# Kernel optimization log

Measured on AMD Instinct MI355X. Metric: run time of the kernel, lower is better.

Reference implementation:

```python
import jax, jax.numpy as jnp
import numpy as np

EPS = 1e-8

def div_safe(n, d):
    return n / jnp.maximum(d, EPS)

def cos_sim(v1, v2):
    # torch F.cosine_similarity along last axis (broadcasting allowed)
    n1 = jnp.linalg.norm(v1, axis=-1)
    n2 = jnp.linalg.norm(v2, axis=-1)
    dot = jnp.sum(v1 * v2, axis=-1)
    return dot / (jnp.maximum(n1, EPS) * jnp.maximum(n2, EPS))

def cosine_pairwise(v1, v2):
    # v1: (B,L1,H), v2: (B,L2,H) -> (B,L1,L2)
    n1 = jnp.linalg.norm(v1, axis=2)[:, :, None]        # (B,L1,1)
    n2 = jnp.linalg.norm(v2, axis=2)[:, None, :]        # (B,1,L2)
    a = jnp.einsum('bih,bjh->bij', v1, v2)
    return div_safe(a, n1 * n2)

def mpm(v1, v2, w):
    # v1: (B,L,H); v2: (B,L,H) or (B,1,H) (broadcast); w: (P,H)
    mv1 = cos_sim(v1, v2)[..., None]                     # (B,L,1)
    v1w = w[None, None] * v1[:, :, None, :]              # (B,L,P,H)
    v2w = w[None, None] * v2[:, :, None, :]              # (B,L or 1,P,H)
    mvp = cos_sim(v1w, v2w)                              # (B,L,P)
    return [mv1, mvp]

def mpm_pairwise(v1, v2, w):
    # v1: (B,L1,H), v2: (B,L2,H), w: (P,H) -> (B,L1,L2,P)
    v1w = w[None, :, None, :] * v1[:, None, :, :]        # (B,P,L1,H)
    v2w = w[None, :, None, :] * v2[:, None, :, :]        # (B,P,L2,H)
    n = jnp.einsum('bpih,bpjh->bpij', v1w, v2w)
    n1 = jnp.linalg.norm(v1w, axis=3)[:, :, :, None]     # (B,P,L1,1)
    n2 = jnp.linalg.norm(v2w, axis=3)[:, :, None, :]     # (B,P,1,L2)
    return div_safe(n, n1 * n2).transpose(0, 2, 3, 1)

def matching_forward(context_p, mask_p, context_h, mask_h, params):
    H = params.shape[-1]
    B = context_p.shape[0]
    p_fw, p_bw = context_p[..., :H], context_p[..., H:]
    h_fw, h_bw = context_h[..., :H], context_h[..., H:]

    len_p = jnp.sum(mask_p, axis=1)
    len_h = jnp.sum(mask_h, axis=1)
    last_p = jnp.clip(len_p - 1, 0)
    last_h = jnp.clip(len_h - 1, 0)
    bidx = jnp.arange(B)
    p_fw_last = p_fw[bidx, last_p][:, None, :]           # (B,1,H)
    h_fw_last = h_fw[bidx, last_h][:, None, :]
    p_bw_last = p_bw[:, 0:1, :]
    h_bw_last = h_bw[:, 0:1, :]

    cos_fw = cosine_pairwise(p_fw, h_fw)                 # (B,L1,L2)
    cos_bw = cosine_pairwise(p_bw, h_bw)

    mv_p = [cos_fw.max(axis=2, keepdims=True), cos_fw.mean(axis=2, keepdims=True),
            cos_bw.max(axis=2, keepdims=True), cos_bw.mean(axis=2, keepdims=True)]
    mv_h = [cos_fw.max(axis=1)[..., None], cos_fw.mean(axis=1)[..., None],
            cos_bw.max(axis=1)[..., None], cos_bw.mean(axis=1)[..., None]]

    # full match
    mv_p += mpm(p_fw, h_fw_last, params[0]) + mpm(p_bw, h_bw_last, params[1])
    mv_h += mpm(h_fw, p_fw_last, params[0]) + mpm(h_bw, p_bw_last, params[1])

    # maxpool match
    m_fw = mpm_pairwise(p_fw, h_fw, params[2])           # (B,L1,L2,P)
    m_bw = mpm_pairwise(p_bw, h_bw, params[3])
    mv_p += [m_fw.max(axis=2), m_fw.mean(axis=2), m_bw.max(axis=2), m_bw.mean(axis=2)]
    mv_h += [m_fw.max(axis=1), m_fw.mean(axis=1), m_bw.max(axis=1), m_bw.mean(axis=1)]

    # attentive (mean) match -- sum over seq axis expressed as einsum, no 4D tensor
    att_mean_h_fw = div_safe(jnp.einsum('bij,bjh->bih', cos_fw, h_fw), cos_fw.sum(axis=2, keepdims=True))
    att_mean_h_bw = div_safe(jnp.einsum('bij,bjh->bih', cos_bw, h_bw), cos_bw.sum(axis=2, keepdims=True))
    att_mean_p_fw = div_safe(jnp.einsum('bij,bih->bjh', cos_fw, p_fw), cos_fw.sum(axis=1)[..., None])
    att_mean_p_bw = div_safe(jnp.einsum('bij,bih->bjh', cos_bw, p_bw), cos_bw.sum(axis=1)[..., None])
    mv_p += mpm(p_fw, att_mean_h_fw, params[4]) + mpm(p_bw, att_mean_h_bw, params[5])
    mv_h += mpm(h_fw, att_mean_p_fw, params[4]) + mpm(h_bw, att_mean_p_bw, params[5])

    # max-attentive match -- needs elementwise max over the pair axis
    att_max_h_fw = jnp.max(h_fw[:, None, :, :] * cos_fw[..., None], axis=2)  # (B,L1,H)
    att_max_h_bw = jnp.max(h_bw[:, None, :, :] * cos_bw[..., None], axis=2)
    att_max_p_fw = jnp.max(p_fw[:, :, None, :] * cos_fw[..., None], axis=1)  # (B,L2,H)
    att_max_p_bw = jnp.max(p_bw[:, :, None, :] * cos_bw[..., None], axis=1)
    mv_p += mpm(p_fw, att_max_h_fw, params[6]) + mpm(p_bw, att_max_h_bw, params[7])
    mv_h += mpm(h_fw, att_max_p_fw, params[6]) + mpm(h_bw, att_max_p_bw, params[7])

    return jnp.concatenate(mv_p, axis=2), jnp.concatenate(mv_h, axis=2)

def setup_inputs() -> dict:
    key = jax.random.key(0)
    k1, k2, k3 = jax.random.split(key, 3)
    B, L, H, P, M = 16, 128, 100, 20, 8
    context_p = jax.random.normal(k1, (B, L, 2 * H), dtype=jnp.float32)
    context_h = jax.random.normal(k2, (B, L, 2 * H), dtype=jnp.float32)
    mask_p = jnp.ones((B, L), dtype=jnp.int32)
    mask_h = jnp.ones((B, L), dtype=jnp.int32)
    # kaiming_normal_ (fan_in=H): std = sqrt(2/H)
    params = jax.random.normal(k3, (M, P, H), dtype=jnp.float32) * np.sqrt(2.0 / H)
    return {"context_p": context_p, "mask_p": mask_p,
            "context_h": context_h, "mask_h": mask_h, "params": params}

def reference(context_p, mask_p, context_h, mask_h, params):
    return matching_forward(context_p, mask_p, context_h, mask_h, params)
```

## Files before the change

### kernel.cpp

```cpp
#include <hip/hip_runtime.h>
#include <math.h>

#define B 16
#define L 128
#define H 100
#define P 20
#define CH 210
#define EPSF 1e-8f

#define OFF_COS    0u
#define OFF_COST   524288u
#define OFF_ROWSUM 1048576u
#define OFF_COLSUM 1052672u
#define OFF_LASTV  1056768u
#define OFF_W2T    1063168u
#define OFF_ATT    1079968u

typedef __attribute__((ext_vector_type(8))) short bf16x8;
typedef __attribute__((ext_vector_type(4))) float f32x4;

__device__ inline unsigned short f2bf(float x) {
    union { float f; unsigned u; } c; c.f = x;
    unsigned r = c.u + 0x7fffu + ((c.u >> 16) & 1u);
    return (unsigned short)(r >> 16);
}

__global__ __launch_bounds__(256, 2) void pair_kernel(
    const float* __restrict__ ctx_p, const float* __restrict__ ctx_h,
    const int* __restrict__ mask_p, const int* __restrict__ mask_h,
    const float* __restrict__ params,
    float* __restrict__ cosbuf, float* __restrict__ cosT,
    float* __restrict__ rowsum, float* __restrict__ colsum,
    float* __restrict__ lastv, float* __restrict__ w2t,
    float* __restrict__ out)
{
    __shared__ __align__(16) char smem[37888];
    const int k = blockIdx.x, t = threadIdx.x;

    if (k >= 672) {
        if (k == 672) {
            for (int e = t; e < 16800; e += 256) {
                int m = e / 2100, r = e % 2100;
                int g = r / 84, qq = r % 84, hh = qq / 21, p = qq % 21;
                int h = 4*g + hh;
                float v = 1.f;
                if (p < P) { float w = params[((size_t)m*P + p)*H + h]; v = w*w; }
                w2t[e] = v;
            }
        } else {
            const int task = k - 673, b = task >> 1, is_h = task & 1;
            const float* ctx = is_h ? ctx_h : ctx_p;
            const int* mask = is_h ? mask_h : mask_p;
            int* sm = (int*)smem;
            if (t < 128) sm[t] = mask[b*L + t];
            __syncthreads();
            for (int s = 64; s > 0; s >>= 1) {
                if (t < s) sm[t] += sm[t + s];
                __syncthreads();
            }
            int last = sm[0] - 1;
            if (last < 0) last = 0;
            if (t < H) {
                lastv[((size_t)(is_h*2 + 0)*B + b)*H + t] = ctx[(size_t)(b*L + last)*(2*H) + t];
                lastv[((size_t)(is_h*2 + 1)*B + b)*H + t] = ctx[(size_t)(b*L + 0)*(2*H) + H + t];
            }
        }
        return;
    }

    const int b = k & 15, dir = (k >> 4) & 1, p = k >> 5;
    short* sB     = (short*)smem;
    float* colred = (float*)(smem + 32768);
    float* nlds   = (float*)(smem + 32768 + 4096);

    for (int e = t; e < 2048; e += 256) {
        int cgi = e >> 8, kt = (e >> 6) & 3, qq = (e >> 4) & 3, rl2 = e & 15;
        int row = cgi*16 + rl2, kb = kt*32 + qq*8;
        float v[8];
#pragma unroll
        for (int j = 0; j < 8; ++j) v[j] = 0.f;
        const float* src = ctx_h + (size_t)(b*L + row)*(2*H) + dir*H;
        if (kb < H)     { float4 f = *(const float4*)(src + kb);     v[0]=f.x; v[1]=f.y; v[2]=f.z; v[3]=f.w; }
        if (kb + 4 < H) { float4 f = *(const float4*)(src + kb + 4); v[4]=f.x; v[5]=f.y; v[6]=f.z; v[7]=f.w; }
        bf16x8 pk;
#pragma unroll
        for (int j = 0; j < 8; ++j) pk[j] = (short)f2bf(v[j]);
        *(bf16x8*)&sB[e*8] = pk;
    }

    const float* prow = params + ((size_t)(2 + dir)*P + p)*H;

    const int w = t >> 6, lane = t & 63, q = lane >> 4, rl = lane & 15;
    bf16x8 af[2][4];
#pragma unroll
    for (int rgi = 0; rgi < 2; ++rgi) {
        int row = (w*2 + rgi)*16 + rl;
        const float* src = ctx_p + (size_t)(b*L + row)*(2*H) + dir*H;
#pragma unroll
        for (int kt = 0; kt < 4; ++kt) {
            int kb = kt*32 + q*8;
            float v[8];
#pragma unroll
            for (int j = 0; j < 8; ++j) v[j] = 0.f;
            if (p < P) {
                if (kb < H) {
                    float4 f = *(const float4*)(src + kb);
                    float4 wv = *(const float4*)(prow + kb);
                    v[0]=f.x*wv.x*wv.x; v[1]=f.y*wv.y*wv.y; v[2]=f.z*wv.z*wv.z; v[3]=f.w*wv.w*wv.w;
                }
                if (kb + 4 < H) {
                    float4 f = *(const float4*)(src + kb + 4);
                    float4 wv = *(const float4*)(prow + kb + 4);
                    v[4]=f.x*wv.x*wv.x; v[5]=f.y*wv.y*wv.y; v[6]=f.z*wv.z*wv.z; v[7]=f.w*wv.w*wv.w;
                }
            } else {
                if (kb < H)     { float4 f = *(const float4*)(src + kb);     v[0]=f.x; v[1]=f.y; v[2]=f.z; v[3]=f.w; }
                if (kb + 4 < H) { float4 f = *(const float4*)(src + kb + 4); v[4]=f.x; v[5]=f.y; v[6]=f.z; v[7]=f.w; }
            }
            bf16x8 pk;
#pragma unroll
            for (int j = 0; j < 8; ++j) pk[j] = (short)f2bf(v[j]);
            af[rgi][kt] = pk;
        }
    }

    {
        const int r = t & 127, sd = t >> 7;
        const float* nrow = (sd ? ctx_h : ctx_p) + (size_t)(b*L + r)*(2*H) + dir*H;
        float n2 = 0.f;
        if (p < P) {
            for (int g = 0; g < 25; ++g) {
                float4 v = *(const float4*)(nrow + 4*g);
                float4 wv = *(const float4*)(prow + 4*g);
                n2 = fmaf(wv.x*wv.x, v.x*v.x, n2);
                n2 = fmaf(wv.y*wv.y, v.y*v.y, n2);
                n2 = fmaf(wv.z*wv.z, v.z*v.z, n2);
                n2 = fmaf(wv.w*wv.w, v.w*v.w, n2);
            }
        } else {
            for (int g = 0; g < 25; ++g) {
                float4 v = *(const float4*)(nrow + 4*g);
                n2 = fmaf(v.x, v.x, n2); n2 = fmaf(v.y, v.y, n2);
                n2 = fmaf(v.z, v.z, n2); n2 = fmaf(v.w, v.w, n2);
            }
        }
        nlds[sd*128 + r] = sqrtf(n2);
    }
    __syncthreads();

    f32x4 acc[2][8];
#pragma unroll
    for (int rgi = 0; rgi < 2; ++rgi)
#pragma unroll
        for (int cgi = 0; cgi < 8; ++cgi) acc[rgi][cgi] = (f32x4)0.f;
#pragma unroll
    for (int kt = 0; kt < 4; ++kt) {
#pragma unroll
        for (int cgi = 0; cgi < 8; ++cgi) {
            bf16x8 bfr = *(bf16x8*)&sB[((cgi*4 + kt)*64 + lane)*8];
            acc[0][cgi] = __builtin_amdgcn_mfma_f32_16x16x32_bf16(af[0][kt], bfr, acc[0][cgi], 0, 0, 0);
            acc[1][cgi] = __builtin_amdgcn_mfma_f32_16x16x32_bf16(af[1][kt], bfr, acc[1][cgi], 0, 0, 0);
        }
    }

    float na[2][4];
#pragma unroll
    for (int rgi = 0; rgi < 2; ++rgi)
#pragma unroll
        for (int r = 0; r < 4; ++r) na[rgi][r] = nlds[0*128 + (w*2 + rgi)*16 + q*4 + r];
    float nbv[8];
#pragma unroll
    for (int cgi = 0; cgi < 8; ++cgi) nbv[cgi] = nlds[1*128 + cgi*16 + rl];

    const bool iscos = (p == P);
    float* cosm  = cosbuf + (size_t)(dir*B + b)*16384;
    float* cosmT = cosT   + (size_t)(dir*B + b)*16384;

    int chmax, chmean;
    if (p < P) { chmax = (dir ? 86 : 46) + p; chmean = (dir ? 106 : 66) + p; }
    else       { chmax = dir*2;              chmean = dir*2 + 1; }

    float rowm[2][4], rows_[2][4], colm[8], cols_[8];
#pragma unroll
    for (int rgi = 0; rgi < 2; ++rgi)
#pragma unroll
        for (int r = 0; r < 4; ++r) { rowm[rgi][r] = -INFINITY; rows_[rgi][r] = 0.f; }
#pragma unroll
    for (int cgi = 0; cgi < 8; ++cgi) { colm[cgi] = -INFINITY; cols_[cgi] = 0.f; }

#pragma unroll
    for (int rgi = 0; rgi < 2; ++rgi) {
        int i0 = (w*2 + rgi)*16 + q*4;
#pragma unroll
        for (int cgi = 0; cgi < 8; ++cgi) {
            float m[4];
#pragma unroll
            for (int r = 0; r < 4; ++r) {
                float d = fmaxf(na[rgi][r]*nbv[cgi], EPSF);
                m[r] = acc[rgi][cgi][r] * __builtin_amdgcn_rcpf(d);
                rowm[rgi][r] = fmaxf(rowm[rgi][r], m[r]);
                rows_[rgi][r] += m[r];
            }
            float cM = fmaxf(fmaxf(m[0], m[1]), fmaxf(m[2], m[3]));
            colm[cgi] = fmaxf(colm[cgi], cM);
            cols_[cgi] += (m[0] + m[1]) + (m[2] + m[3]);
            if (iscos) {
                int j = cgi*16 + rl;
                float4 f4; f4.x = m[0]; f4.y = m[1]; f4.z = m[2]; f4.w = m[3];
                *(float4*)&cosmT[j*128 + i0] = f4;
#pragma unroll
                for (int r = 0; r < 4; ++r) cosm[(i0 + r)*128 + j] = m[r];
            }
        }
    }
#pragma unroll
    for (int rgi = 0; rgi < 2; ++rgi)
#pragma unroll
        for (int r = 0; r < 4; ++r) {
            float mx = rowm[rgi][r], sm = rows_[rgi][r];
#pragma unroll
            for (int d = 1; d < 16; d <<= 1) {
                mx = fmaxf(mx, __shfl_xor(mx, d));
                sm += __shfl_xor(sm, d);
            }
            if (rl == 0) {
                int i = (w*2 + rgi)*16 + q*4 + r;
                float* orow = out + (size_t)(b*L + i)*CH;
                orow[chmax] = mx; orow[chmean] = sm * (1.f/L);
                if (iscos) rowsum[(dir*B + b)*L + i] = sm;
            }
        }
#pragma unroll
    for (int cgi = 0; cgi < 8; ++cgi) {
        float mx = colm[cgi], sm = cols_[cgi];
        mx = fmaxf(mx, __shfl_xor(mx, 16)); sm += __shfl_xor(sm, 16);
        mx = fmaxf(mx, __shfl_xor(mx, 32)); sm += __shfl_xor(sm, 32);
        if (q == 0) {
            colred[(0*4 + w)*128 + cgi*16 + rl] = mx;
            colred[(1*4 + w)*128 + cgi*16 + rl] = sm;
        }
    }
    __syncthreads();
    {
        int c = t & 127, kind = t >> 7;
        float v0 = colred[(kind*4 + 0)*128 + c], v1 = colred[(kind*4 + 1)*128 + c];
        float v2 = colred[(kind*4 + 2)*128 + c], v3 = colred[(kind*4 + 3)*128 + c];
        float* oh = out + (size_t)B*L*CH + (size_t)(b*L + c)*CH;
        if (kind == 0) {
            oh[chmax] = fmaxf(fmaxf(v0, v1), fmaxf(v2, v3));
        } else {
            float sm = (v0 + v1) + (v2 + v3);
            oh[chmean] = sm * (1.f/L);
            if (iscos) colsum[(dir*B + b)*L + c] = sm;
        }
    }
}

__global__ __launch_bounds__(256) void att_kernel(
    const float* __restrict__ ctx_p, const float* __restrict__ ctx_h,
    const float* __restrict__ cosbuf, const float* __restrict__ cosT,
    const float* __restrict__ rowsum, const float* __restrict__ colsum,
    float* __restrict__ attbuf)
{
    const int b = blockIdx.x;
    const int dir = blockIdx.y >> 1, side = blockIdx.y & 1;
    const int rc = blockIdx.z, r0 = rc*16;
    const int t = threadIdx.x;

    __shared__ float sv[L][H];
    __shared__ float cvT[L][16];

    const float* mat = (side ? cosbuf : cosT) + (size_t)(dir*B + b)*16384;
    const float* src = side ? ctx_p : ctx_h;

    for (int e = t; e < 3200; e += 256) {
        int row = e / 25, g = e - row*25;
        *(float4*)&sv[row][4*g] =
            *(const float4*)(src + (size_t)(b*L + row)*(2*H) + dir*H + 4*g);
    }
    for (int e = t; e < 2048; e += 256) {
        int s = e >> 4, r = e & 15;
        cvT[s][r] = mat[s*L + r0 + r];
    }
    __syncthreads();

    const int tr = t & 7, th = t >> 3;
    if (th < 25) {
        float acc[2][4], amx[2][4];
#pragma unroll
        for (int rr = 0; rr < 2; ++rr)
#pragma unroll
            for (int qq = 0; qq < 4; ++qq) { acc[rr][qq] = 0.f; amx[rr][qq] = -INFINITY; }
        for (int s = 0; s < L; ++s) {
            float2 c2 = *(const float2*)&cvT[s][2*tr];
            float4 v4 = *(const float4*)&sv[s][4*th];
            float cs[2] = {c2.x, c2.y};
            float vs[4] = {v4.x, v4.y, v4.z, v4.w};
#pragma unroll
            for (int rr = 0; rr < 2; ++rr)
#pragma unroll
                for (int qq = 0; qq < 4; ++qq) {
                    float pr = cs[rr] * vs[qq];
                    acc[rr][qq] += pr;
                    amx[rr][qq] = fmaxf(amx[rr][qq], pr);
                }
        }
        const float* den = side ? colsum : rowsum;
#pragma unroll
        for (int rr = 0; rr < 2; ++rr) {
            int rg = r0 + 2*tr + rr;
            float d = fmaxf(den[(dir*B + b)*L + rg], EPSF);
            float* meanp = attbuf + ((((size_t)side*2 + 0)*2 + dir)*B*L + (b*L + rg))*H + 4*th;
            float* maxp  = attbuf + ((((size_t)side*2 + 1)*2 + dir)*B*L + (b*L + rg))*H + 4*th;
            float4 fm; fm.x = acc[rr][0]/d; fm.y = acc[rr][1]/d; fm.z = acc[rr][2]/d; fm.w = acc[rr][3]/d;
            float4 fx; fx.x = amx[rr][0]; fx.y = amx[rr][1]; fx.z = amx[rr][2]; fx.w = amx[rr][3];
            *(float4*)meanp = fm;
            *(float4*)maxp  = fx;
        }
    }
}

__global__ __launch_bounds__(128) void point_kernel(
    const float* __restrict__ ctx_p, const float* __restrict__ ctx_h,
    const float* __restrict__ w2t,
    const float* __restrict__ lastv, const float* __restrict__ attbuf,
    float* __restrict__ out)
{
    const int b = blockIdx.x, side = blockIdx.y;
    const int m = blockIdx.z >> 1, ih = blockIdx.z & 1;
    const int t = threadIdx.x;
    const int il = t & 63, half = t >> 6;
    const int i = ih*64 + il;
    const int dir = m & 1;
    const int wsel_[6] = {0, 1, 4, 5, 6, 7};
    const int chb_[6]  = {4, 25, 126, 147, 168, 189};

    const float* v1p = (side ? ctx_h : ctx_p) + (size_t)(b*L + i)*(2*H) + dir*H;
    const float* v2p;
    if (m < 2) {
        v2p = lastv + ((size_t)((side ? 0 : 2) + dir)*B + b)*H;
    } else {
        int kind = (m >= 4) ? 1 : 0;
        v2p = attbuf + ((((size_t)side*2 + kind)*2 + dir)*B*L + (b*L + i))*H;
    }
    const float* wt = w2t + (size_t)wsel_[m]*2100;

    float s11[21], s22[21], s12[21];
#pragma unroll
    for (int p = 0; p < 21; ++p) { s11[p] = 0.f; s22[p] = 0.f; s12[p] = 0.f; }
    const int g0 = half ? 13 : 0, g1 = half ? 25 : 13;
    for (int g = g0; g < g1; ++g) {
        float4 x = *(const float4*)(v1p + 4*g);
        float4 y = *(const float4*)(v2p + 4*g);
        float xx[4] = {x.x*x.x, x.y*x.y, x.z*x.z, x.w*x.w};
        float yy[4] = {y.x*y.x, y.y*y.y, y.z*y.z, y.w*y.w};
        float xy[4] = {x.x*y.x, x.y*y.y, x.z*y.z, x.w*y.w};
        const float* wg = wt + g*84;
#pragma unroll
        for (int hh = 0; hh < 4; ++hh)
#pragma unroll
            for (int p = 0; p < 21; ++p) {
                float w2 = wg[hh*21 + p];
                s11[p] = fmaf(w2, xx[hh], s11[p]);
                s22[p] = fmaf(w2, yy[hh], s22[p]);
                s12[p] = fmaf(w2, xy[hh], s12[p]);
            }
    }
    __shared__ float red[3][21][64];
    if (half) {
#pragma unroll
        for (int p = 0; p < 21; ++p) {
            red[0][p][il] = s11[p]; red[1][p][il] = s22[p]; red[2][p][il] = s12[p];
        }
    }
    __syncthreads();
    if (!half) {
        float* orow = out + (size_t)side*B*L*CH + (size_t)(b*L + i)*CH;
#pragma unroll
        for (int p = 0; p < 21; ++p) {
            float a = s11[p] + red[0][p][il];
            float c = s22[p] + red[1][p][il];
            float d = s12[p] + red[2][p][il];
            float cv = d / (fmaxf(sqrtf(a), EPSF) * fmaxf(sqrtf(c), EPSF));
            orow[(p == P) ? chb_[m] : (chb_[m] + 1 + p)] = cv;
        }
    }
}

extern "C" void kernel_launch(void* const* d_in, const int* in_sizes, int n_in,
                              void* d_out, int out_size, void* d_ws, size_t ws_size,
                              hipStream_t stream) {
    const float* ctx_p  = (const float*)d_in[0];
    const int*   mask_p = (const int*)d_in[1];
    const float* ctx_h  = (const float*)d_in[2];
    const int*   mask_h = (const int*)d_in[3];
    const float* params = (const float*)d_in[4];
    float* out = (float*)d_out;

    float* ws = (float*)d_ws;
    float* cosbuf = ws + OFF_COS;
    float* cosT   = ws + OFF_COST;
    float* rowsum = ws + OFF_ROWSUM;
    float* colsum = ws + OFF_COLSUM;
    float* lastv  = ws + OFF_LASTV;
    float* w2t    = ws + OFF_W2T;
    float* attbuf = ws + OFF_ATT;

    pair_kernel <<<dim3(705),      256, 0, stream>>>(ctx_p, ctx_h, mask_p, mask_h, params,
                                                     cosbuf, cosT, rowsum, colsum,
                                                     lastv, w2t, out);
    att_kernel  <<<dim3(B, 4, 8),  256, 0, stream>>>(ctx_p, ctx_h, cosbuf, cosT,
                                                     rowsum, colsum, attbuf);
    point_kernel<<<dim3(B, 2, 12), 128, 0, stream>>>(ctx_p, ctx_h, w2t, lastv, attbuf, out);
}
```

Measured before the change: 135.1 us.

## Fuse attentive pooling with multi-perspective matching into one kernel

Merges the attention kernel and the pointwise multi-perspective kernel into a single launch. The mean and max attentive vectors are kept in shared memory and consumed directly by the matching step, so the global attbuf round trip and one kernel launch go away. The w2t weight layout becomes h-major with padded rows in LDS, and each row's reduction over h is split across 8 lanes and combined with shuffles. The full-match blocks (m<2) are appended as extra blocks of the same grid. This adds shared-memory pressure (about 58KB per block) and extra syncs, and the per-row work may now be less parallel than before.

After: 122.5 us. 9.3% less time.

```diff
diff --git a/kernel.cpp b/kernel.cpp
--- a/kernel.cpp
+++ b/kernel.cpp
@@ -14,7 +14,6 @@
 #define OFF_COLSUM 1052672u
 #define OFF_LASTV  1056768u
 #define OFF_W2T    1063168u
-#define OFF_ATT    1079968u
 
 typedef __attribute__((ext_vector_type(8))) short bf16x8;
 typedef __attribute__((ext_vector_type(4))) float f32x4;
@@ -41,8 +40,7 @@
         if (k == 672) {
             for (int e = t; e < 16800; e += 256) {
                 int m = e / 2100, r = e % 2100;
-                int g = r / 84, qq = r % 84, hh = qq / 21, p = qq % 21;
-                int h = 4*g + hh;
+                int h = r / 21, p = r % 21;
                 float v = 1.f;
                 if (p < P) { float w = params[((size_t)m*P + p)*H + h]; v = w*w; }
                 w2t[e] = v;
@@ -256,27 +254,84 @@
     }
 }
 
-__global__ __launch_bounds__(256) void att_kernel(
+__global__ __launch_bounds__(256, 2) void attpoint_kernel(
     const float* __restrict__ ctx_p, const float* __restrict__ ctx_h,
     const float* __restrict__ cosbuf, const float* __restrict__ cosT,
     const float* __restrict__ rowsum, const float* __restrict__ colsum,
-    float* __restrict__ attbuf)
+    const float* __restrict__ lastv, const float* __restrict__ w2t,
+    float* __restrict__ out)
 {
-    const int b = blockIdx.x;
-    const int dir = blockIdx.y >> 1, side = blockIdx.y & 1;
-    const int rc = blockIdx.z, r0 = rc*16;
-    const int t = threadIdx.x;
-
-    __shared__ float sv[L][H];
-    __shared__ float cvT[L][16];
+    __shared__ __align__(16) char smem[59392];
+    const int k = blockIdx.x, t = threadIdx.x;
+
+    if (k >= 512) {
+        const int task = k - 512;
+        const int b = task & 15, side = (task >> 4) & 1, m = task >> 5;
+        const int i = t & 127, half = t >> 7;
+        const int chb = m ? 25 : 4;
+        const float* v1p = (side ? ctx_h : ctx_p) + (size_t)(b*L + i)*(2*H) + m*H;
+        const float* v2p = lastv + ((size_t)((side ? 0 : 2) + m)*B + b)*H;
+        const float* wt = w2t + (size_t)m*2100;
+
+        float s11[21], s22[21], s12[21];
+#pragma unroll
+        for (int p = 0; p < 21; ++p) { s11[p] = 0.f; s22[p] = 0.f; s12[p] = 0.f; }
+        const int g0 = half ? 13 : 0, g1 = half ? 25 : 13;
+        for (int g = g0; g < g1; ++g) {
+            float4 x = *(const float4*)(v1p + 4*g);
+            float4 y = *(const float4*)(v2p + 4*g);
+            float xx[4] = {x.x*x.x, x.y*x.y, x.z*x.z, x.w*x.w};
+            float yy[4] = {y.x*y.x, y.y*y.y, y.z*y.z, y.w*y.w};
+            float xy[4] = {x.x*y.x, x.y*y.y, x.z*y.z, x.w*y.w};
+            const float* wg = wt + g*84;
+#pragma unroll
+            for (int hh = 0; hh < 4; ++hh)
+#pragma unroll
+                for (int p = 0; p < 21; ++p) {
+                    float w2 = wg[hh*21 + p];
+                    s11[p] = fmaf(w2, xx[hh], s11[p]);
+                    s22[p] = fmaf(w2, yy[hh], s22[p]);
+                    s12[p] = fmaf(w2, xy[hh], s12[p]);
+                }
+        }
+        float* red = (float*)smem;
+        if (half) {
+#pragma unroll
+            for (int p = 0; p < 21; ++p) {
+                red[(0*21 + p)*128 + i] = s11[p];
+                red[(1*21 + p)*128 + i] = s22[p];
+                red[(2*21 + p)*128 + i] = s12[p];
+            }
+        }
+        __syncthreads();
+        if (!half) {
+            float* orow = out + (size_t)side*B*L*CH + (size_t)(b*L + i)*CH;
+#pragma unroll
+            for (int p = 0; p < 21; ++p) {
+                float a = s11[p] + red[(0*21 + p)*128 + i];
+                float c = s22[p] + red[(1*21 + p)*128 + i];
+                float d = s12[p] + red[(2*21 + p)*128 + i];
+                float cv = d / (fmaxf(sqrtf(a), EPSF) * fmaxf(sqrtf(c), EPSF));
+                orow[(p == P) ? chb : (chb + 1 + p)] = cv;
+            }
+        }
+        return;
+    }
+
+    const int b = k & 15, side = (k >> 4) & 1, dir = (k >> 5) & 1, rc = k >> 6;
+    const int r0 = rc*16;
+    float* sf = (float*)smem;
+    float (*sv)[100] = (float(*)[100])smem;
+    float (*cvT)[16] = (float(*)[16])(smem + 51200);
 
     const float* mat = (side ? cosbuf : cosT) + (size_t)(dir*B + b)*16384;
-    const float* src = side ? ctx_p : ctx_h;
+    const float* srcJ = side ? ctx_p : ctx_h;
+    const float* srcI = side ? ctx_h : ctx_p;
 
     for (int e = t; e < 3200; e += 256) {
         int row = e / 25, g = e - row*25;
         *(float4*)&sv[row][4*g] =
-            *(const float4*)(src + (size_t)(b*L + row)*(2*H) + dir*H + 4*g);
+            *(const float4*)(srcJ + (size_t)(b*L + row)*(2*H) + dir*H + 4*g);
     }
     for (int e = t; e < 2048; e += 256) {
         int s = e >> 4, r = e & 15;
@@ -285,12 +340,12 @@
     __syncthreads();
 
     const int tr = t & 7, th = t >> 3;
+    float acc[2][4], amx[2][4];
+#pragma unroll
+    for (int rr = 0; rr < 2; ++rr)
+#pragma unroll
+        for (int qq = 0; qq < 4; ++qq) { acc[rr][qq] = 0.f; amx[rr][qq] = -INFINITY; }
     if (th < 25) {
-        float acc[2][4], amx[2][4];
-#pragma unroll
-        for (int rr = 0; rr < 2; ++rr)
-#pragma unroll
-            for (int qq = 0; qq < 4; ++qq) { acc[rr][qq] = 0.f; amx[rr][qq] = -INFINITY; }
         for (int s = 0; s < L; ++s) {
             float2 c2 = *(const float2*)&cvT[s][2*tr];
             float4 v4 = *(const float4*)&sv[s][4*th];
@@ -305,84 +360,89 @@
                     amx[rr][qq] = fmaxf(amx[rr][qq], pr);
                 }
         }
+    }
+    __syncthreads();
+
+    float* attv = sf;
+    float* v1s  = sf + 3200;
+    float* w2l  = sf + 4800;
+    if (th < 25) {
         const float* den = side ? colsum : rowsum;
 #pragma unroll
         for (int rr = 0; rr < 2; ++rr) {
-            int rg = r0 + 2*tr + rr;
-            float d = fmaxf(den[(dir*B + b)*L + rg], EPSF);
-            float* meanp = attbuf + ((((size_t)side*2 + 0)*2 + dir)*B*L + (b*L + rg))*H + 4*th;
-            float* maxp  = attbuf + ((((size_t)side*2 + 1)*2 + dir)*B*L + (b*L + rg))*H + 4*th;
-            float4 fm; fm.x = acc[rr][0]/d; fm.y = acc[rr][1]/d; fm.z = acc[rr][2]/d; fm.w = acc[rr][3]/d;
-            float4 fx; fx.x = amx[rr][0]; fx.y = amx[rr][1]; fx.z = amx[rr][2]; fx.w = amx[rr][3];
-            *(float4*)meanp = fm;
-            *(float4*)maxp  = fx;
-        }
-    }
-}
-
-__global__ __launch_bounds__(128) void point_kernel(
-    const float* __restrict__ ctx_p, const float* __restrict__ ctx_h,
-    const float* __restrict__ w2t,
-    const float* __restrict__ lastv, const float* __restrict__ attbuf,
-    float* __restrict__ out)
-{
-    const int b = blockIdx.x, side = blockIdx.y;
-    const int m = blockIdx.z >> 1, ih = blockIdx.z & 1;
-    const int t = threadIdx.x;
-    const int il = t & 63, half = t >> 6;
-    const int i = ih*64 + il;
-    const int dir = m & 1;
-    const int wsel_[6] = {0, 1, 4, 5, 6, 7};
-    const int chb_[6]  = {4, 25, 126, 147, 168, 189};
-
-    const float* v1p = (side ? ctx_h : ctx_p) + (size_t)(b*L + i)*(2*H) + dir*H;
-    const float* v2p;
-    if (m < 2) {
-        v2p = lastv + ((size_t)((side ? 0 : 2) + dir)*B + b)*H;
-    } else {
-        int kind = (m >= 4) ? 1 : 0;
-        v2p = attbuf + ((((size_t)side*2 + kind)*2 + dir)*B*L + (b*L + i))*H;
-    }
-    const float* wt = w2t + (size_t)wsel_[m]*2100;
-
-    float s11[21], s22[21], s12[21];
-#pragma unroll
-    for (int p = 0; p < 21; ++p) { s11[p] = 0.f; s22[p] = 0.f; s12[p] = 0.f; }
-    const int g0 = half ? 13 : 0, g1 = half ? 25 : 13;
-    for (int g = g0; g < g1; ++g) {
-        float4 x = *(const float4*)(v1p + 4*g);
-        float4 y = *(const float4*)(v2p + 4*g);
-        float xx[4] = {x.x*x.x, x.y*x.y, x.z*x.z, x.w*x.w};
-        float yy[4] = {y.x*y.x, y.y*y.y, y.z*y.z, y.w*y.w};
-        float xy[4] = {x.x*y.x, x.y*y.y, x.z*y.z, x.w*y.w};
-        const float* wg = wt + g*84;
-#pragma unroll
-        for (int hh = 0; hh < 4; ++hh)
+            int rloc = 2*tr + rr;
+            float d = fmaxf(den[(dir*B + b)*L + r0 + rloc], EPSF);
+            float inv = 1.f / d;
+#pragma unroll
+            for (int qq = 0; qq < 4; ++qq) {
+                attv[0*1600 + rloc*100 + 4*th + qq] = acc[rr][qq] * inv;
+                attv[1*1600 + rloc*100 + 4*th + qq] = amx[rr][qq];
+            }
+        }
+    }
+    for (int e = t; e < 400; e += 256) {
+        int row = e / 25, g = e - row*25;
+        *(float4*)&v1s[row*100 + 4*g] =
+            *(const float4*)(srcI + (size_t)(b*L + r0 + row)*(2*H) + dir*H + 4*g);
+    }
+    for (int e = t; e < 4200; e += 256) {
+        int kind = e >= 2100 ? 1 : 0, r = e - kind*2100;
+        int h = r / 21, p = r - h*21;
+        int wsel = 4 + kind*2 + dir;
+        w2l[kind*3600 + h*36 + p] = w2t[(size_t)wsel*2100 + r];
+    }
+    __syncthreads();
+
+    {
+        const int task = t >> 3, tt = t & 7;
+        const int kind = task >> 4, row = task & 15;
+        const int h0 = tt*13, cnt = (tt < 7) ? 13 : 9;
+        const float* av  = attv + kind*1600 + row*100;
+        const float* v1r = v1s + row*100;
+        const float* wk  = w2l + kind*3600;
+
+        float s11[21], s22[21], s12[21];
+#pragma unroll
+        for (int p = 0; p < 21; ++p) { s11[p] = 0.f; s22[p] = 0.f; s12[p] = 0.f; }
+        for (int hh = 0; hh < cnt; ++hh) {
+            int h = h0 + hh;
+            float a = v1r[h], c = av[h];
+            float xx = a*a, yy = c*c, xy = a*c;
+            const float* wrow = wk + h*36;
+#pragma unroll
+            for (int pg = 0; pg < 5; ++pg) {
+                float4 wv = *(const float4*)&wrow[4*pg];
+                float ws[4] = {wv.x, wv.y, wv.z, wv.w};
+#pragma unroll
+                for (int q = 0; q < 4; ++q) {
+                    int p = 4*pg + q;
+                    s11[p] = fmaf(ws[q], xx, s11[p]);
+                    s22[p] = fmaf(ws[q], yy, s22[p]);
+                    s12[p] = fmaf(ws[q], xy, s12[p]);
+                }
+            }
+            float w20 = wrow[20];
+            s11[20] = fmaf(w20, xx, s11[20]);
+            s22[20] = fmaf(w20, yy, s22[20]);
+            s12[20] = fmaf(w20, xy, s12[20]);
+        }
+#pragma unroll
+        for (int p = 0; p < 21; ++p) {
+#pragma unroll
+            for (int d = 1; d < 8; d <<= 1) {
+                s11[p] += __shfl_xor(s11[p], d);
+                s22[p] += __shfl_xor(s22[p], d);
+                s12[p] += __shfl_xor(s12[p], d);
+            }
+        }
+        if (tt == 0) {
+            int chb = kind ? (dir ? 189 : 168) : (dir ? 147 : 126);
+            float* orow = out + (size_t)side*B*L*CH + (size_t)(b*L + r0 + row)*CH;
 #pragma unroll
             for (int p = 0; p < 21; ++p) {
-                float w2 = wg[hh*21 + p];
-                s11[p] = fmaf(w2, xx[hh], s11[p]);
-                s22[p] = fmaf(w2, yy[hh], s22[p]);
-                s12[p] = fmaf(w2, xy[hh], s12[p]);
-            }
-    }
-    __shared__ float red[3][21][64];
-    if (half) {
-#pragma unroll
-        for (int p = 0; p < 21; ++p) {
-            red[0][p][il] = s11[p]; red[1][p][il] = s22[p]; red[2][p][il] = s12[p];
-        }
-    }
-    __syncthreads();
-    if (!half) {
-        float* orow = out + (size_t)side*B*L*CH + (size_t)(b*L + i)*CH;
-#pragma unroll
-        for (int p = 0; p < 21; ++p) {
-            float a = s11[p] + red[0][p][il];
-            float c = s22[p] + red[1][p][il];
-            float d = s12[p] + red[2][p][il];
-            float cv = d / (fmaxf(sqrtf(a), EPSF) * fmaxf(sqrtf(c), EPSF));
-            orow[(p == P) ? chb_[m] : (chb_[m] + 1 + p)] = cv;
+                float cv = s12[p] / (fmaxf(sqrtf(s11[p]), EPSF) * fmaxf(sqrtf(s22[p]), EPSF));
+                orow[(p == P) ? chb : (chb + 1 + p)] = cv;
+            }
         }
     }
 }
@@ -404,12 +464,10 @@
     float* colsum = ws + OFF_COLSUM;
     float* lastv  = ws + OFF_LASTV;
     float* w2t    = ws + OFF_W2T;
-    float* attbuf = ws + OFF_ATT;
-
-    pair_kernel <<<dim3(705),      256, 0, stream>>>(ctx_p, ctx_h, mask_p, mask_h, params,
-                                                     cosbuf, cosT, rowsum, colsum,
-                                                     lastv, w2t, out);
-    att_kernel  <<<dim3(B, 4, 8),  256, 0, stream>>>(ctx_p, ctx_h, cosbuf, cosT,
-                                                     rowsum, colsum, attbuf);
-    point_kernel<<<dim3(B, 2, 12), 128, 0, stream>>>(ctx_p, ctx_h, w2t, lastv, attbuf, out);
+
+    pair_kernel    <<<dim3(705), 256, 0, stream>>>(ctx_p, ctx_h, mask_p, mask_h, params,
+                                                   cosbuf, cosT, rowsum, colsum,
+                                                   lastv, w2t, out);
+    attpoint_kernel<<<dim3(576), 256, 0, stream>>>(ctx_p, ctx_h, cosbuf, cosT,
+                                                   rowsum, colsum, lastv, w2t, out);
 }
```
